# Optimization experiments

Measured on AMD Instinct MI355X. Metric: run time of the kernel, lower is better.

Reference implementation:

```python
import jax, jax.numpy as jnp
import numpy as np

RGB_MEAN = jnp.array([0.4488, 0.4371, 0.404], dtype=jnp.float32)
RGB_RANGE = 255.0
N_FEATS = 64
N_RESBLOCKS = 16
SUPER_OUT = 100 * 16  # full SuperConv2d out_channels
RES_SCALE = 1.0


def conv2d(x, w, b):
    # x: [N,C,H,W], w: [O,I,3,3], SAME padding (pad=1)
    y = jax.lax.conv_general_dilated(
        x, w, window_strides=(1, 1), padding='SAME',
        dimension_numbers=('NCHW', 'OIHW', 'NCHW'))
    return y + b[None, :, None, None]


def setup_inputs() -> dict:
    key = jax.random.key(0)
    ks = jax.random.split(key, 12)
    N, C, H, W = 8, 3, 128, 128
    nf, nrb = N_FEATS, N_RESBLOCKS
    sd = 0.05  # weight std to keep activations bounded over 16 resblocks
    inp = {
        'x': jax.random.normal(ks[0], (N, C, H, W), jnp.float32) * 50.0 + 127.0,
        'head_w': jax.random.normal(ks[1], (nf, C, 3, 3), jnp.float32) * sd,
        'head_b': jnp.zeros((nf,), jnp.float32),
        'rb_w1': jax.random.normal(ks[2], (nrb, nf, nf, 3, 3), jnp.float32) * sd,
        'rb_b1': jnp.zeros((nrb, nf), jnp.float32),
        'rb_w2': jax.random.normal(ks[3], (nrb, nf, nf, 3, 3), jnp.float32) * sd,
        'rb_b2': jnp.zeros((nrb, nf), jnp.float32),
        'body_w': jax.random.normal(ks[4], (nf, nf, 3, 3), jnp.float32) * sd,
        'body_b': jnp.zeros((nf,), jnp.float32),
        'super_w': jax.random.normal(ks[5], (SUPER_OUT, nf, 3, 3), jnp.float32) * sd,
        'super_b': jnp.zeros((SUPER_OUT,), jnp.float32),
        'out_w': jax.random.normal(ks[6], (3, 100, 3, 3), jnp.float32) * sd,
        'out_b': jnp.zeros((3,), jnp.float32),
        'scale': 2,
    }
    return inp


def reference(x, head_w, head_b, rb_w1, rb_b1, rb_w2, rb_b2,
              body_w, body_b, super_w, super_b, out_w, out_b, scale):
    s = int(scale)
    mean = (RGB_RANGE * RGB_MEAN)[None, :, None, None]
    x = x - mean  # sub_mean (std = 1)
    h = conv2d(x, head_w, head_b)  # head: [N,64,H,W]

    def resblock(carry, params):
        w1, b1, w2, b2 = params
        r = jax.nn.relu(conv2d(carry, w1, b1))
        r = conv2d(r, w2, b2)
        return carry + RES_SCALE * r, None

    res, _ = jax.lax.scan(resblock, h, (rb_w1, rb_b1, rb_w2, rb_b2))
    res = conv2d(res, body_w, body_b)
    res = res + h

    # SuperConv2d: dynamic out channels = scale^2 * 100 (slice of full weight)
    out_nc = s * s * 100
    t = conv2d(res, super_w[:out_nc], super_b[:out_nc])  # [N, 100*s^2, H, W]

    # pixel_shuffle: out[i,j,k] = in[i//s, j//s, k*s^2 + (i%s)*s + (j%s)]
    # == standard depth-to-space with channel group ordering (k, a, b)
    N, _, H, W = t.shape
    t = t.reshape(N, 100, s, s, H, W)          # [N,100,a,b,H,W]
    t = t.transpose(0, 1, 4, 2, 5, 3)          # [N,100,H,a,W,b]
    t = t.reshape(N, 100, H * s, W * s)

    y = conv2d(t, out_w, out_b)                # [N,3,H*s,W*s]
    y = y + mean  # add_mean
    return y
```

## Files before the change

kernel.cpp:

```cpp
#include <hip/hip_runtime.h>
#include <hip/hip_bf16.h>

#define HH 128
#define WW 128

typedef _Float16 half2_t __attribute__((ext_vector_type(2)));
typedef _Float16 half4_t __attribute__((ext_vector_type(4)));
typedef _Float16 half8 __attribute__((ext_vector_type(8)));
typedef float f32x4 __attribute__((ext_vector_type(4)));

__global__ __launch_bounds__(256)
void wxform_k(const float* __restrict__ rb_w1, const float* __restrict__ rb_w2,
              const float* __restrict__ body_w, const float* __restrict__ super_w,
              const float* __restrict__ out_w,
              _Float16* __restrict__ Wt, _Float16* __restrict__ Wo) {
    const int per64 = 64 * 64 * 9;
    const int n64   = 33 * per64;
    const int nW    = n64 + 448 * 64 * 9;
    const int total = nW + 1350;
    for (int i = blockIdx.x * 256 + threadIdx.x; i < total; i += gridDim.x * 256) {
        if (i < n64) {
            int l  = i / per64;
            int r  = i - l * per64;
            int ic = r & 63, oc = (r >> 6) & 63, tap = r >> 12;
            const float* src = (l < 16) ? (rb_w1 + (size_t)l * per64)
                             : (l < 32) ? (rb_w2 + (size_t)(l - 16) * per64)
                                        : body_w;
            Wt[i] = (_Float16)src[(oc * 64 + ic) * 9 + tap];
        } else if (i < nW) {
            int r   = i - n64;
            int ic  = r & 63;
            int oc  = (r >> 6) % 448;
            int tap = (r >> 6) / 448;
            float v = (oc < 400) ? super_w[((size_t)oc * 64 + ic) * 9 + tap] : 0.f;
            Wt[i] = (_Float16)v;
        } else {
            int j = i - nW;
            int c = j / 450, r = j - c * 450;
            int p = r / 9, tap = r - p * 9;
            Wo[j * 2]     = (_Float16)out_w[(c * 100 + 2 * p) * 9 + tap];
            Wo[j * 2 + 1] = (_Float16)out_w[(c * 100 + 2 * p + 1) * 9 + tap];
        }
    }
}

__global__ __launch_bounds__(256)
void head_k(const float* __restrict__ x, const float* __restrict__ w,
            const float* __restrict__ b, _Float16* __restrict__ out) {
    int n  = blockIdx.z;
    int gx = blockIdx.x * 16 + (threadIdx.x & 15);
    int gy = blockIdx.y * 16 + (threadIdx.x >> 4);
    float msub[3] = {255.0f * 0.4488f, 255.0f * 0.4371f, 255.0f * 0.4040f};
    float iv[27];
#pragma unroll
    for (int c = 0; c < 3; ++c)
#pragma unroll
        for (int dy = 0; dy < 3; ++dy)
#pragma unroll
            for (int dx = 0; dx < 3; ++dx) {
                int yy = gy + dy - 1, xx = gx + dx - 1;
                float v = 0.f;
                if ((unsigned)yy < HH && (unsigned)xx < WW)
                    v = x[(((size_t)n * 3 + c) * HH + yy) * WW + xx] - msub[c];
                iv[c * 9 + dy * 3 + dx] = v;
            }
    for (int ocg = 0; ocg < 16; ++ocg) {
        half4_t o;
#pragma unroll
        for (int q = 0; q < 4; ++q) {
            int oc  = ocg * 4 + q;
            float a = b[oc];
#pragma unroll
            for (int t = 0; t < 27; ++t) a = fmaf(iv[t], w[oc * 27 + t], a);
            o[q] = (_Float16)a;
        }
        *(half4_t*)&out[((((size_t)n * 16 + ocg) * HH + gy) * WW + gx) * 4] = o;
    }
}

__global__ __launch_bounds__(256, 2)
void frb1_k(const _Float16* __restrict__ in, const _Float16* __restrict__ W1,
            const _Float16* __restrict__ W2, const float* __restrict__ b1,
            const float* __restrict__ b2, _Float16* __restrict__ out) {
    __shared__ __align__(16) _Float16 sBuf[18432 + 18432];
    _Float16* sIn  = sBuf;
    _Float16* sMid = sBuf;
    _Float16* sW   = sBuf + 18432;

    int tid = threadIdx.x;
    int bx = blockIdx.x, by = blockIdx.y, n = blockIdx.z;
    int wv = tid >> 6, lane = tid & 63;
    int lx = lane & 15, lg = lane >> 4;
    int o0 = wv * 4 - 1;
    int g2 = wv & 1;
    int hh = wv >> 1;

    half8 pf[9];
#define PF_W(Wsrc, h)                                                         \
    _Pragma("unroll")                                                         \
    for (int j = 0; j < 9; ++j) {                                             \
        int i = tid + 256 * j;                                                \
        int g = i & 3, oc = (i >> 2) & 63, tap = i >> 8;                      \
        pf[j] = *(const half8*)&Wsrc[(size_t)(tap * 64 + oc) * 64 + (h) * 32 + g * 8]; \
    }
#define WR_W()                                                                \
    _Pragma("unroll")                                                         \
    for (int j = 0; j < 9; ++j) {                                             \
        int i = tid + 256 * j;                                                \
        int g = i & 3, oc = (i >> 2) & 63, tap = i >> 8;                      \
        *(half8*)&sW[(tap * 32 + (oc >> 1)) * 64 +                            \
                     (((g + (oc & 1) * 4) ^ ((oc >> 1) & 7)) << 3)] = pf[j];  \
    }
#define RD_A(tap, oc)                                                         \
    (*(const half8*)&sW[((tap) * 32 + ((oc) >> 1)) * 64 +                     \
                        (((lg + ((oc) & 1) * 4) ^ (((oc) >> 1) & 7)) << 3)])

    PF_W(W1, 0)
    for (int i = tid; i < 2304; i += 256) {
        int icg = i / 288, pl = i - icg * 288;
        int py = pl / 18, px = pl - py * 18;
        int gy = by * 12 + py - 2, gx = bx * 14 + px - 2;
        half8 v = {0, 0, 0, 0, 0, 0, 0, 0};
        if ((unsigned)gy < (unsigned)HH && (unsigned)gx < (unsigned)WW) {
            size_t base = ((((size_t)n * 16 + icg * 2) * HH + gy) * WW + gx) * 4;
            half4_t a = *(const half4_t*)&in[base];
            half4_t c = *(const half4_t*)&in[base + (size_t)HH * WW * 4];
            v[0] = a[0]; v[1] = a[1]; v[2] = a[2]; v[3] = a[3];
            v[4] = c[0]; v[5] = c[1]; v[6] = c[2]; v[7] = c[3];
        }
        *(half8*)&sIn[pl * 64 + ((icg ^ (pl & 7)) << 3)] = v;
    }
    WR_W()
    __syncthreads();

    f32x4 acc1[4][4];
#pragma unroll
    for (int r = 0; r < 4; ++r)
#pragma unroll
        for (int t = 0; t < 4; ++t) acc1[r][t] = (f32x4){0.f, 0.f, 0.f, 0.f};

#define CONV1_CHUNK(h)                                                        \
    {                                                                         \
        _Pragma("unroll")                                                     \
        for (int dx = 0; dx < 3; ++dx) {                                      \
            half8 Bf[6];                                                      \
            _Pragma("unroll")                                                 \
            for (int d = 0; d < 6; ++d) {                                     \
                int pl = (o0 + d + 1) * 18 + (lx + dx);                       \
                Bf[d] = *(const half8*)&sIn[pl * 64 + ((((h) * 4 + lg) ^ (pl & 7)) << 3)]; \
            }                                                                 \
            _Pragma("unroll")                                                 \
            for (int dy = 0; dy < 3; ++dy) {                                  \
                int tap = dy * 3 + dx;                                        \
                half8 Af[4];                                                  \
                _Pragma("unroll")                                             \
                for (int t = 0; t < 4; ++t) Af[t] = RD_A(tap, t * 16 + lx);   \
                _Pragma("unroll")                                             \
                for (int r = 0; r < 4; ++r)                                   \
                    _Pragma("unroll")                                         \
                    for (int t = 0; t < 4; ++t)                               \
                        acc1[r][t] = __builtin_amdgcn_mfma_f32_16x16x32_f16(  \
                            Af[t], Bf[r + dy], acc1[r][t], 0, 0, 0);          \
            }                                                                 \
        }                                                                     \
    }

    PF_W(W1, 1)
    CONV1_CHUNK(0)
    __syncthreads();
    WR_W()
    __syncthreads();
    PF_W(W2, 0)
    CONV1_CHUNK(1)
    half4_t rs[6][2];
#pragma unroll
    for (int r = 0; r < 6; ++r)
#pragma unroll
        for (int t = 0; t < 2; ++t) {
            int oc0 = hh * 32 + t * 16 + lg * 4;
            int pl  = (g2 * 6 + r + 2) * 18 + lx + 2;
            rs[r][t] = *(const half4_t*)&sIn[pl * 64 + (((oc0 >> 3) ^ (pl & 7)) << 3) + (oc0 & 4)];
        }
    __syncthreads();

    {
        int gcol = bx * 14 + lx - 1;
        bool colok = (unsigned)gcol < (unsigned)WW;
#pragma unroll
        for (int r = 0; r < 4; ++r) {
            int o    = o0 + r;
            int grow = by * 12 + o;
            bool ok  = colok && ((unsigned)grow < (unsigned)HH);
#pragma unroll
            for (int t = 0; t < 4; ++t) {
                int oc0 = t * 16 + lg * 4;
                f32x4 bv = *(const f32x4*)&b1[oc0];
                int pl2 = (o + 1) * 18 + lx;
                half4_t ov;
#pragma unroll
                for (int q = 0; q < 4; ++q)
                    ov[q] = ok ? (_Float16)fmaxf(acc1[r][t][q] + bv[q], 0.f)
                               : (_Float16)0.f;
                *(half4_t*)&sMid[pl2 * 64 + (((oc0 >> 3) ^ (pl2 & 7)) << 3) + (oc0 & 4)] = ov;
            }
        }
    }
    WR_W()
    __syncthreads();

    f32x4 acc2[6][2];
#pragma unroll
    for (int r = 0; r < 6; ++r)
#pragma unroll
        for (int t = 0; t < 2; ++t) acc2[r][t] = (f32x4){0.f, 0.f, 0.f, 0.f};

#define CONV2_CHUNK(h)                                                        \
    {                                                                         \
        _Pragma("unroll")                                                     \
        for (int dx = 0; dx < 3; ++dx) {                                      \
            half8 Bf[8];                                                      \
            _Pragma("unroll")                                                 \
            for (int d = 0; d < 8; ++d) {                                     \
                int pl = (g2 * 6 + d) * 18 + (lx + dx);                       \
                Bf[d] = *(const half8*)&sMid[pl * 64 + ((((h) * 4 + lg) ^ (pl & 7)) << 3)]; \
            }                                                                 \
            _Pragma("unroll")                                                 \
            for (int dy = 0; dy < 3; ++dy) {                                  \
                int tap = dy * 3 + dx;                                        \
                half8 Af[2];                                                  \
                _Pragma("unroll")                                             \
                for (int t = 0; t < 2; ++t) Af[t] = RD_A(tap, hh * 32 + t * 16 + lx); \
                _Pragma("unroll")                                             \
                for (int r = 0; r < 6; ++r)                                   \
                    _Pragma("unroll")                                         \
                    for (int t = 0; t < 2; ++t)                               \
                        acc2[r][t] = __builtin_amdgcn_mfma_f32_16x16x32_f16(  \
                            Af[t], Bf[r + dy], acc2[r][t], 0, 0, 0);          \
            }                                                                 \
        }                                                                     \
    }

    PF_W(W2, 1)
    CONV2_CHUNK(0)
    __syncthreads();
    WR_W()
    __syncthreads();
    CONV2_CHUNK(1)
    {
        int gcol = bx * 14 + lx;
        bool sok = (lx < 14) && (gcol < WW);
#pragma unroll
        for (int r = 0; r < 6; ++r) {
            int y = by * 12 + g2 * 6 + r;
            if (!sok || y >= HH) continue;
#pragma unroll
            for (int t = 0; t < 2; ++t) {
                int oc0 = hh * 32 + t * 16 + lg * 4;
                f32x4 bv = *(const f32x4*)&b2[oc0];
                size_t gi = ((((size_t)n * 16 + (oc0 >> 2)) * HH + y) * WW + gcol) * 4;
                half4_t ov;
#pragma unroll
                for (int q = 0; q < 4; ++q)
                    ov[q] = (_Float16)(acc2[r][t][q] + bv[q] + (float)rs[r][t][q]);
                *(half4_t*)&out[gi] = ov;
            }
        }
    }
#undef PF_W
#undef WR_W
#undef RD_A
#undef CONV1_CHUNK
#undef CONV2_CHUNK
}

template<bool RES, bool NT>
__global__ __launch_bounds__(512, 2)
void mconv_k(const _Float16* __restrict__ in, const _Float16* __restrict__ Wt,
             const float* __restrict__ bias, const _Float16* __restrict__ resid,
             _Float16* __restrict__ out, int OCp, int OCr, int C4) {
    __shared__ __align__(16) _Float16 sIn[18 * 18 * 64];
    __shared__ __align__(16) _Float16 sW[9 * 32 * 64];

    int tid = threadIdx.x;
    int n = blockIdx.z, bx = blockIdx.x, by = blockIdx.y;

    for (int i = tid; i < 2592; i += 512) {
        int icg = i / 324, pl = i - icg * 324;
        int py = pl / 18, px = pl - py * 18;
        int gy = by * 16 + py - 1, gx = bx * 16 + px - 1;
        half8 v = {0, 0, 0, 0, 0, 0, 0, 0};
        if ((unsigned)gy < (unsigned)HH && (unsigned)gx < (unsigned)WW) {
            size_t base = ((((size_t)n * 16 + icg * 2) * HH + gy) * WW + gx) * 4;
            half4_t a = *(const half4_t*)&in[base];
            half4_t c = *(const half4_t*)&in[base + (size_t)HH * WW * 4];
            v[0] = a[0]; v[1] = a[1]; v[2] = a[2]; v[3] = a[3];
            v[4] = c[0]; v[5] = c[1]; v[6] = c[2]; v[7] = c[3];
        }
        *(half8*)&sIn[pl * 64 + ((icg ^ (pl & 7)) << 3)] = v;
    }
    __syncthreads();

    int wv = tid >> 6, lane = tid & 63;
    int lx = lane & 15, lg = lane >> 4;
    int r0 = wv * 2;
    int gx0 = bx * 16 + lx;

    for (int ocb = 0; ocb < OCp; ocb += 32) {
        __syncthreads();
        for (int i = tid; i < 2304; i += 512) {
            int tap = i >> 8, oc = (i >> 3) & 31, icg = i & 7;
            half8 v = *(const half8*)&Wt[((size_t)(tap * OCp + ocb + oc)) * 64 + icg * 8];
            *(half8*)&sW[(tap * 32 + oc) * 64 + ((icg ^ (oc & 7)) << 3)] = v;
        }
        __syncthreads();

        f32x4 acc[2][2];
#pragma unroll
        for (int r = 0; r < 2; ++r)
#pragma unroll
            for (int t = 0; t < 2; ++t) acc[r][t] = (f32x4){0.f, 0.f, 0.f, 0.f};

#pragma unroll
        for (int icstep = 0; icstep < 2; ++icstep) {
            int icg = icstep * 4 + lg;
#pragma unroll
            for (int dx = 0; dx < 3; ++dx) {
                half8 Bf[4];
#pragma unroll
                for (int d = 0; d < 4; ++d) {
                    int pl = (r0 + d) * 18 + lx + dx;
                    Bf[d] = *(const half8*)&sIn[pl * 64 + ((icg ^ (pl & 7)) << 3)];
                }
#pragma unroll
                for (int dy = 0; dy < 3; ++dy) {
                    int tap = dy * 3 + dx;
                    half8 Af[2];
#pragma unroll
                    for (int t = 0; t < 2; ++t) {
                        int oc = t * 16 + lx;
                        Af[t] = *(const half8*)&sW[(tap * 32 + oc) * 64 + ((icg ^ (oc & 7)) << 3)];
                    }
#pragma unroll
                    for (int r = 0; r < 2; ++r)
#pragma unroll
                        for (int t = 0; t < 2; ++t)
                            acc[r][t] = __builtin_amdgcn_mfma_f32_16x16x32_f16(
                                Af[t], Bf[r + dy], acc[r][t], 0, 0, 0);
                }
            }
        }
#pragma unroll
        for (int r = 0; r < 2; ++r) {
            int y = by * 16 + r0 + r;
#pragma unroll
            for (int t = 0; t < 2; ++t) {
                int oc0 = ocb + t * 16 + lg * 4;
                if (oc0 >= OCr) continue;
                f32x4 bv = *(const f32x4*)&bias[oc0];
                size_t gi = ((((size_t)n * C4 + (oc0 >> 2)) * HH + y) * WW + gx0) * 4;
                float vv[4];
#pragma unroll
                for (int q = 0; q < 4; ++q) vv[q] = acc[r][t][q] + bv[q];
                if (RES) {
                    half4_t rg = *(const half4_t*)&resid[gi];
#pragma unroll
                    for (int q = 0; q < 4; ++q) vv[q] += (float)rg[q];
                }
                half4_t o;
#pragma unroll
                for (int q = 0; q < 4; ++q) o[q] = (_Float16)vv[q];
                if (NT) __builtin_nontemporal_store(o, (half4_t*)&out[gi]);
                else    *(half4_t*)&out[gi] = o;
            }
        }
    }
}

__global__ __launch_bounds__(256)
void out_k(const _Float16* __restrict__ S, const _Float16* __restrict__ Wo,
           const float* __restrict__ b, float* __restrict__ out) {
    __shared__ __align__(16) _Float16 sG[5 * 324 * 8];
    int n = blockIdx.z;
    int tid = threadIdx.x;
    int ty = tid >> 4, tx = tid & 15;
    int a  = blockIdx.y * 16 + ty;
    int bc = blockIdx.x * 16 + tx;
    float acc[3][2][2];
#pragma unroll
    for (int c = 0; c < 3; ++c)
#pragma unroll
        for (int oy = 0; oy < 2; ++oy)
#pragma unroll
            for (int ox = 0; ox < 2; ++ox) acc[c][oy][ox] = 0.f;

    for (int ch = 0; ch < 10; ++ch) {
        __syncthreads();
        for (int i = tid; i < 1620; i += 256) {
            int p = i / 324, pl = i - p * 324;
            int py = pl / 18, px = pl - py * 18;
            int Y = blockIdx.y * 16 + py - 1, X = blockIdx.x * 16 + px - 1;
            half4_t va = {0, 0, 0, 0}, vc = {0, 0, 0, 0};
            if ((unsigned)Y < 128u && (unsigned)X < 128u) {
                size_t base = ((((size_t)n * 100 + ch * 10 + p * 2) * 128 + Y) * 128 + X) * 4;
                va = *(const half4_t*)&S[base];
                vc = *(const half4_t*)&S[base + (size_t)128 * 128 * 4];
            }
            half8 v;
            v[0] = va[0]; v[1] = vc[0]; v[2] = va[1]; v[3] = vc[1];
            v[4] = va[2]; v[5] = vc[2]; v[6] = va[3]; v[7] = vc[3];
            *(half8*)&sG[(p * 324 + pl) * 8] = v;
        }
        __syncthreads();
#pragma unroll
        for (int p = 0; p < 5; ++p) {
            half2_t wv[3][9];
#pragma unroll
            for (int c = 0; c < 3; ++c)
#pragma unroll
                for (int t = 0; t < 9; ++t)
                    wv[c][t] = *(const half2_t*)&Wo[((c * 50 + ch * 5 + p) * 9 + t) * 2];
            half8 G[3][3];
#pragma unroll
            for (int yi = 0; yi < 3; ++yi)
#pragma unroll
                for (int xi = 0; xi < 3; ++xi)
                    G[yi][xi] = *(const half8*)&sG[(p * 324 + (ty + yi) * 18 + tx + xi) * 8];
#pragma unroll
            for (int oy = 0; oy < 2; ++oy)
#pragma unroll
                for (int ox = 0; ox < 2; ++ox)
#pragma unroll
                    for (int dy = 0; dy < 3; ++dy)
#pragma unroll
                        for (int dx = 0; dx < 3; ++dx) {
                            const int ey = oy + dy - 1, ex = ox + dx - 1;
                            const int yi = (ey >> 1) + 1, xi = (ex >> 1) + 1;
                            const int sub = (ey & 1) * 2 + (ex & 1);
                            half8 g8 = G[yi][xi];
                            half2_t gp = {g8[2 * sub], g8[2 * sub + 1]};
#pragma unroll
                            for (int c = 0; c < 3; ++c)
                                acc[c][oy][ox] = __builtin_amdgcn_fdot2(
                                    gp, wv[c][dy * 3 + dx], acc[c][oy][ox], false);
                        }
        }
    }
    const float madd[3] = {255.0f * 0.4488f, 255.0f * 0.4371f, 255.0f * 0.4040f};
#pragma unroll
    for (int c = 0; c < 3; ++c)
#pragma unroll
        for (int oy = 0; oy < 2; ++oy)
#pragma unroll
            for (int ox = 0; ox < 2; ++ox)
                out[(((size_t)n * 3 + c) * 256 + 2 * a + oy) * 256 + 2 * bc + ox] =
                    acc[c][oy][ox] + b[c] + madd[c];
}

extern "C" void kernel_launch(void* const* d_in, const int* in_sizes, int n_in,
                              void* d_out, int out_size, void* d_ws, size_t ws_size,
                              hipStream_t stream) {
    const float* x       = (const float*)d_in[0];
    const float* head_w  = (const float*)d_in[1];
    const float* head_b  = (const float*)d_in[2];
    const float* rb_w1   = (const float*)d_in[3];
    const float* rb_b1   = (const float*)d_in[4];
    const float* rb_w2   = (const float*)d_in[5];
    const float* rb_b2   = (const float*)d_in[6];
    const float* body_w  = (const float*)d_in[7];
    const float* body_b  = (const float*)d_in[8];
    const float* super_w = (const float*)d_in[9];
    const float* super_b = (const float*)d_in[10];
    const float* out_w   = (const float*)d_in[11];
    const float* out_b   = (const float*)d_in[12];
    float* out = (float*)d_out;

    const size_t ACT = (size_t)16777216;
    char* wsb = (char*)d_ws;
    _Float16* Tb = (_Float16*)wsb;
    _Float16* Hb = (_Float16*)(wsb + ACT);
    _Float16* Cb = (_Float16*)(wsb + 2 * ACT);
    _Float16* Sb = (_Float16*)(wsb + ACT);
    _Float16* Wt = (_Float16*)(wsb + ACT + 104857600);
    _Float16* Wo = (_Float16*)(wsb + ACT + 104857600 + 2949120);

    wxform_k<<<dim3(1440), 256, 0, stream>>>(rb_w1, rb_w2, body_w, super_w,
                                             out_w, Wt, Wo);

    head_k<<<dim3(8, 8, 8), 256, 0, stream>>>(x, head_w, head_b, Hb);

    const _Float16* Wt_bod = Wt + (size_t)32 * 36864;
    const _Float16* Wt_sup = Wt + (size_t)33 * 36864;

    const _Float16* cur = Hb;
    for (int i = 0; i < 16; ++i) {
        _Float16* dst = (i & 1) ? Cb : Tb;
        frb1_k<<<dim3(10, 11, 8), 256, 0, stream>>>(
            cur, Wt + (size_t)i * 36864, Wt + (size_t)(16 + i) * 36864,
            rb_b1 + i * 64, rb_b2 + i * 64, dst);
        cur = dst;
    }
    mconv_k<true, false><<<dim3(8, 8, 8), 512, 0, stream>>>(
        Cb, Wt_bod, body_b, Hb, Tb, 64, 64, 16);
    mconv_k<false, true><<<dim3(8, 8, 8), 512, 0, stream>>>(
        Tb, Wt_sup, super_b, nullptr, Sb, 448, 400, 100);
    out_k<<<dim3(8, 8, 8), 256, 0, stream>>>(Sb, Wo, out_b, out);
}
```

Baseline: 874.0 us.

## Split out_k input channels across two thread halves with smaller spatial tiles

The final output convolution now uses 8x16 spatial tiles, giving twice as many blocks. Within each block the 256 threads form two halves that process disjoint halves of the 50 channel pairs, and their partial sums are combined through shared memory at the end. This is meant to raise the number of resident waves and the parallelism of a small kernel that had few blocks. In exchange the halo overhead per tile grows (10 rows loaded for 8 output rows) and an extra shared-memory reduction step is added.

```diff
diff --git a/kernel.cpp b/kernel.cpp
--- a/kernel.cpp
+++ b/kernel.cpp
@@ -379,11 +379,13 @@
 __global__ __launch_bounds__(256)
 void out_k(const _Float16* __restrict__ S, const _Float16* __restrict__ Wo,
            const float* __restrict__ b, float* __restrict__ out) {
-    __shared__ __align__(16) _Float16 sG[5 * 324 * 8];
+    __shared__ __align__(16) _Float16 sG[10 * 180 * 8];
     int n = blockIdx.z;
     int tid = threadIdx.x;
-    int ty = tid >> 4, tx = tid & 15;
-    int a  = blockIdx.y * 16 + ty;
+    int h   = tid >> 7;
+    int pix = tid & 127;
+    int ty = pix >> 4, tx = pix & 15;
+    int a  = blockIdx.y * 8 + ty;
     int bc = blockIdx.x * 16 + tx;
     float acc[3][2][2];
 #pragma unroll
@@ -393,38 +395,41 @@
 #pragma unroll
             for (int ox = 0; ox < 2; ++ox) acc[c][oy][ox] = 0.f;
 
-    for (int ch = 0; ch < 10; ++ch) {
+    for (int it = 0; it < 5; ++it) {
         __syncthreads();
-        for (int i = tid; i < 1620; i += 256) {
-            int p = i / 324, pl = i - p * 324;
+        for (int i = tid; i < 1800; i += 256) {
+            int p = i / 180, pl = i - p * 180;
             int py = pl / 18, px = pl - py * 18;
-            int Y = blockIdx.y * 16 + py - 1, X = blockIdx.x * 16 + px - 1;
+            int gp = (p < 5) ? (it * 5 + p) : (25 + it * 5 + (p - 5));
+            int Y = blockIdx.y * 8 + py - 1, X = blockIdx.x * 16 + px - 1;
             half4_t va = {0, 0, 0, 0}, vc = {0, 0, 0, 0};
             if ((unsigned)Y < 128u && (unsigned)X < 128u) {
-                size_t base = ((((size_t)n * 100 + ch * 10 + p * 2) * 128 + Y) * 128 + X) * 4;
+                size_t base = ((((size_t)n * 100 + gp * 2) * 128 + Y) * 128 + X) * 4;
                 va = *(const half4_t*)&S[base];
                 vc = *(const half4_t*)&S[base + (size_t)128 * 128 * 4];
             }
             half8 v;
             v[0] = va[0]; v[1] = vc[0]; v[2] = va[1]; v[3] = vc[1];
             v[4] = va[2]; v[5] = vc[2]; v[6] = va[3]; v[7] = vc[3];
-            *(half8*)&sG[(p * 324 + pl) * 8] = v;
+            *(half8*)&sG[(p * 180 + pl) * 8] = v;
         }
         __syncthreads();
 #pragma unroll
         for (int p = 0; p < 5; ++p) {
+            int sp = h * 5 + p;
+            int gp = h ? (25 + it * 5 + p) : (it * 5 + p);
             half2_t wv[3][9];
 #pragma unroll
             for (int c = 0; c < 3; ++c)
 #pragma unroll
                 for (int t = 0; t < 9; ++t)
-                    wv[c][t] = *(const half2_t*)&Wo[((c * 50 + ch * 5 + p) * 9 + t) * 2];
+                    wv[c][t] = *(const half2_t*)&Wo[((c * 50 + gp) * 9 + t) * 2];
             half8 G[3][3];
 #pragma unroll
             for (int yi = 0; yi < 3; ++yi)
 #pragma unroll
                 for (int xi = 0; xi < 3; ++xi)
-                    G[yi][xi] = *(const half8*)&sG[(p * 324 + (ty + yi) * 18 + tx + xi) * 8];
+                    G[yi][xi] = *(const half8*)&sG[(sp * 180 + (ty + yi) * 18 + tx + xi) * 8];
 #pragma unroll
             for (int oy = 0; oy < 2; ++oy)
 #pragma unroll
@@ -437,23 +442,39 @@
                             const int yi = (ey >> 1) + 1, xi = (ex >> 1) + 1;
                             const int sub = (ey & 1) * 2 + (ex & 1);
                             half8 g8 = G[yi][xi];
-                            half2_t gp = {g8[2 * sub], g8[2 * sub + 1]};
+                            half2_t gp2 = {g8[2 * sub], g8[2 * sub + 1]};
 #pragma unroll
                             for (int c = 0; c < 3; ++c)
                                 acc[c][oy][ox] = __builtin_amdgcn_fdot2(
-                                    gp, wv[c][dy * 3 + dx], acc[c][oy][ox], false);
+                                    gp2, wv[c][dy * 3 + dx], acc[c][oy][ox], false);
                         }
         }
     }
-    const float madd[3] = {255.0f * 0.4488f, 255.0f * 0.4371f, 255.0f * 0.4040f};
-#pragma unroll
-    for (int c = 0; c < 3; ++c)
-#pragma unroll
-        for (int oy = 0; oy < 2; ++oy)
-#pragma unroll
-            for (int ox = 0; ox < 2; ++ox)
-                out[(((size_t)n * 3 + c) * 256 + 2 * a + oy) * 256 + 2 * bc + ox] =
-                    acc[c][oy][ox] + b[c] + madd[c];
+    __syncthreads();
+    float* sR = (float*)sG;
+    if (h == 1) {
+#pragma unroll
+        for (int c = 0; c < 3; ++c)
+#pragma unroll
+            for (int oy = 0; oy < 2; ++oy)
+#pragma unroll
+                for (int ox = 0; ox < 2; ++ox)
+                    sR[pix * 12 + (c * 2 + oy) * 2 + ox] = acc[c][oy][ox];
+    }
+    __syncthreads();
+    if (h == 0) {
+        const float madd[3] = {255.0f * 0.4488f, 255.0f * 0.4371f, 255.0f * 0.4040f};
+#pragma unroll
+        for (int c = 0; c < 3; ++c)
+#pragma unroll
+            for (int oy = 0; oy < 2; ++oy)
+#pragma unroll
+                for (int ox = 0; ox < 2; ++ox) {
+                    float v = acc[c][oy][ox] + sR[pix * 12 + (c * 2 + oy) * 2 + ox];
+                    out[(((size_t)n * 3 + c) * 256 + 2 * a + oy) * 256 + 2 * bc + ox] =
+                        v + b[c] + madd[c];
+                }
+    }
 }
 
 extern "C" void kernel_launch(void* const* d_in, const int* in_sizes, int n_in,
@@ -503,5 +524,5 @@
         Cb, Wt_bod, body_b, Hb, Tb, 64, 64, 16);
     mconv_k<false, true><<<dim3(8, 8, 8), 512, 0, stream>>>(
         Tb, Wt_sup, super_b, nullptr, Sb, 448, 400, 100);
-    out_k<<<dim3(8, 8, 8), 256, 0, stream>>>(Sb, Wo, out_b, out);
+    out_k<<<dim3(8, 16, 8), 256, 0, stream>>>(Sb, Wo, out_b, out);
 }
```

New measurement: 889.9 us. Within noise of the previous version (+1.8%).
